# Kernel optimization log

Measured on AMD Instinct MI355X. Metric: run time of the kernel, lower is better.

Reference implementation:

```python
import jax, jax.numpy as jnp
import numpy as np

NLAYER = 4
H = 0.1


def tv_norm(X, eps=1e-3):
    # mean-center and L2-normalize each channel over the node/edge dim
    X = X - jnp.mean(X, axis=1, keepdims=True)
    return X / jnp.sqrt(jnp.sum(X * X, axis=1, keepdims=True) + eps)


def setup_inputs() -> dict:
    key = jax.random.key(0)
    ks = jax.random.split(key, 12)
    nIn, nopenN, nopenE, nclose = 128, 128, 128, 128
    nN, nE = 50000, 500000
    xn = jax.random.normal(ks[0], (nIn, nN), dtype=jnp.float32)
    xe = jax.random.normal(ks[1], (nIn, nE), dtype=jnp.float32)
    iInd = jax.random.randint(ks[2], (nE,), 0, nN)
    jInd = jax.random.randint(ks[3], (nE,), 0, nN)
    KNopen = jax.random.uniform(ks[4], (nopenN, nIn), dtype=jnp.float32) * 0.1
    KEopen = jax.random.uniform(ks[5], (nopenE, nIn), dtype=jnp.float32) * 0.1
    KNclose = jax.random.uniform(ks[6], (nclose, nopenN), dtype=jnp.float32) * 0.1
    KEclose = jax.random.uniform(ks[7], (nclose, nopenE), dtype=jnp.float32) * 0.1
    KN = jax.random.uniform(ks[8], (NLAYER, nopenE, nopenN), dtype=jnp.float32) * 0.001
    KE = jax.random.uniform(ks[9], (NLAYER, nopenN, nopenE), dtype=jnp.float32) * 0.001
    return {"xn": xn, "xe": xe, "iInd": iInd, "jInd": jInd,
            "KNopen": KNopen, "KEopen": KEopen, "KNclose": KNclose,
            "KEclose": KEclose, "KN": KN, "KE": KE}


def reference(xn, xe, iInd, jInd, KNopen, KEopen, KNclose, KEclose, KN, KE):
    nN = xn.shape[1]

    def node_grad(x):           # [d, nN] -> [d, nE]
        return x[:, iInd] - x[:, jInd]

    def edge_div(e):            # [d, nE] -> [d, nN]
        z = jnp.zeros((e.shape[0], nN), dtype=e.dtype)
        return z.at[:, iInd].add(e).at[:, jInd].add(-e)

    xn = KNopen @ xn            # [nopenN, nN]
    xe = KEopen @ xe            # [nopenE, nE]
    for i in range(NLAYER):
        Ai = tv_norm(KN[i] @ node_grad(xn))          # [nopenE, nE]
        xe = xe + H * jax.nn.relu(Ai)
        Bi = tv_norm(jax.nn.relu(KE[i] @ edge_div(xe)))  # [nopenN, nN]
        xn = xn + H * jax.nn.relu(Bi)
    xn = KNclose @ xn
    xe = KNclose @ xe  # note: original code uses KNclose for xe as well
    return (xn, xe)
```

## Files before the change

kernel.cpp:

```cpp
#include <hip/hip_runtime.h>


#define HSTEP 0.1f
#define TVEPS 1e-3f

typedef __attribute__((ext_vector_type(8))) short short8v;
typedef __attribute__((ext_vector_type(4))) float f32x4;

__device__ inline float4 f4z() { return make_float4(0.f, 0.f, 0.f, 0.f); }

__device__ inline unsigned short f2bf(float x) {
  unsigned u = __float_as_uint(x);
  unsigned r = (u + 0x7fffu + ((u >> 16) & 1u)) >> 16;
  return (unsigned short)r;
}
__device__ inline float bf2f(unsigned short h) {
  return __uint_as_float(((unsigned)h) << 16);
}

__global__ __launch_bounds__(256) void pack6(const float* __restrict__ KNopen,
                                             const float* __restrict__ KEopen,
                                             const float* __restrict__ KN,
                                             unsigned short* __restrict__ dst) {
  const int idx = blockIdx.x * 256 + threadIdx.x;
  const int m = blockIdx.y;
  const int o = idx >> 7, k = idx & 127;
  const float* src;
  if (m == 0) src = KNopen;
  else if (m == 1) src = KEopen;
  else src = KN + (m - 2) * 16384;
  const float val = src[o * 128 + k];
  const unsigned short hi = f2bf(val);
  const unsigned short lo = f2bf(val - bf2f(hi));
  const int lane = (o & 15) + 16 * ((k >> 3) & 3);
  const int base =
      m * 32768 + (k >> 5) * 8192 + (o >> 4) * 512 + lane * 8 + (k & 7);
  dst[base] = hi;
  dst[base + 4096] = lo;
}

__global__ __launch_bounds__(256) void prep_close_w(
    const float* __restrict__ KNclose, const float* __restrict__ KEopen,
    unsigned short* __restrict__ Apack) {
  const int idx = blockIdx.x * 256 + threadIdx.x;
  const int p = idx >> 14, ok = idx & 16383;
  const int o = ok >> 7, k = ok & 127;
  float val;
  if (p == 0) {
    float s = 0.f;
    for (int m = 0; m < 128; ++m)
      s = fmaf(KNclose[o * 128 + m], KEopen[m * 128 + k], s);
    val = s;
  } else {
    val = KNclose[o * 128 + k];
  }
  const unsigned short hi = f2bf(val);
  const unsigned short lo = f2bf(val - bf2f(hi));
  const int chunk = p * 4 + (k >> 5);
  const int lane = (o & 15) + 16 * ((k >> 3) & 3);
  const int base = chunk * 8192 + (o >> 4) * 512 + lane * 8 + (k & 7);
  Apack[base] = hi;
  Apack[base + 4096] = lo;
}

__global__ __launch_bounds__(256, 2) void gemm_e_mfma(
    const float* __restrict__ X, const unsigned short* __restrict__ Wp,
    const int N, float* __restrict__ Yt) {
  __shared__ float4 Asf[1024];
  const int tid = threadIdx.x;
  const int l = tid & 63, w = tid >> 6;
  const int er = l & 15, kg = l >> 4;
  const long e0 = (long)blockIdx.x * 128;

  f32x4 acc[8][2];
#pragma unroll
  for (int of = 0; of < 8; ++of)
#pragma unroll
    for (int f = 0; f < 2; ++f) acc[of][f] = (f32x4){0.f, 0.f, 0.f, 0.f};

  long e_f[2];
  bool ev[2];
#pragma unroll
  for (int f = 0; f < 2; ++f) {
    long e = e0 + 32 * w + 16 * f + er;
    ev[f] = (e < N);
    e_f[f] = ev[f] ? e : (long)(N - 1);
  }

  const short8v* Ap = (const short8v*)Asf;

  for (int ks = 0; ks < 4; ++ks) {
    const float4* src = (const float4*)Wp + ks * 1024;
    __syncthreads();
    Asf[tid] = src[tid];
    Asf[tid + 256] = src[tid + 256];
    Asf[tid + 512] = src[tid + 512];
    Asf[tid + 768] = src[tid + 768];
    __syncthreads();

    short8v bh[2], bl[2];
#pragma unroll
    for (int f = 0; f < 2; ++f) {
      const float* col = X + e_f[f];
      const int kbase = 32 * ks + 8 * kg;
      float xv[8];
#pragma unroll
      for (int j = 0; j < 8; ++j) xv[j] = col[(long)(kbase + j) * N];
#pragma unroll
      for (int j = 0; j < 8; ++j) {
        const unsigned short h = f2bf(xv[j]);
        const unsigned short lo = f2bf(xv[j] - bf2f(h));
        bh[f][j] = (short)h;
        bl[f][j] = (short)lo;
      }
    }

#pragma unroll
    for (int of = 0; of < 8; ++of) {
      const short8v ah = Ap[of * 64 + l];
      const short8v al = Ap[512 + of * 64 + l];
#pragma unroll
      for (int f = 0; f < 2; ++f) {
        acc[of][f] =
            __builtin_amdgcn_mfma_f32_16x16x32_bf16(ah, bh[f], acc[of][f], 0, 0, 0);
        acc[of][f] =
            __builtin_amdgcn_mfma_f32_16x16x32_bf16(ah, bl[f], acc[of][f], 0, 0, 0);
        acc[of][f] =
            __builtin_amdgcn_mfma_f32_16x16x32_bf16(al, bh[f], acc[of][f], 0, 0, 0);
      }
    }
  }

#pragma unroll
  for (int of = 0; of < 8; ++of) {
#pragma unroll
    for (int f = 0; f < 2; ++f) {
      if (!ev[f]) continue;
      *(f32x4*)&Yt[e_f[f] * 128 + of * 16 + 4 * kg] = acc[of][f];
    }
  }
}

template <int MODE>
__global__ __launch_bounds__(256, 2) void gemm_n_mfma(
    const float* __restrict__ X, const unsigned short* __restrict__ Wp,
    const int N, float* __restrict__ Y) {
  __shared__ float4 Asf[1024];
  const int tid = threadIdx.x;
  const int l = tid & 63, w = tid >> 6;
  const int er = l & 15, kg = l >> 4;
  const long n0 = (long)blockIdx.x * 128;

  f32x4 acc[8][2];
#pragma unroll
  for (int of = 0; of < 8; ++of)
#pragma unroll
    for (int f = 0; f < 2; ++f) acc[of][f] = (f32x4){0.f, 0.f, 0.f, 0.f};

  long n_f[2];
  bool nv[2];
#pragma unroll
  for (int f = 0; f < 2; ++f) {
    long n = n0 + 32 * w + 16 * f + er;
    nv[f] = (n < N);
    n_f[f] = nv[f] ? n : (long)(N - 1);
  }

  const short8v* Ap = (const short8v*)Asf;

  for (int ks = 0; ks < 4; ++ks) {
    const float4* src = (const float4*)Wp + ks * 1024;
    __syncthreads();
    Asf[tid] = src[tid];
    Asf[tid + 256] = src[tid + 256];
    Asf[tid + 512] = src[tid + 512];
    Asf[tid + 768] = src[tid + 768];
    __syncthreads();

    short8v bh[2], bl[2];
#pragma unroll
    for (int f = 0; f < 2; ++f) {
      const float* row = X + n_f[f] * 128 + 32 * ks + 8 * kg;
      const float4 v0 = *(const float4*)row;
      const float4 v1 = *(const float4*)(row + 4);
      float xv[8] = {v0.x, v0.y, v0.z, v0.w, v1.x, v1.y, v1.z, v1.w};
#pragma unroll
      for (int j = 0; j < 8; ++j) {
        const unsigned short h = f2bf(xv[j]);
        const unsigned short lo = f2bf(xv[j] - bf2f(h));
        bh[f][j] = (short)h;
        bl[f][j] = (short)lo;
      }
    }

#pragma unroll
    for (int of = 0; of < 8; ++of) {
      const short8v ah = Ap[of * 64 + l];
      const short8v al = Ap[512 + of * 64 + l];
#pragma unroll
      for (int f = 0; f < 2; ++f) {
        acc[of][f] =
            __builtin_amdgcn_mfma_f32_16x16x32_bf16(ah, bh[f], acc[of][f], 0, 0, 0);
        acc[of][f] =
            __builtin_amdgcn_mfma_f32_16x16x32_bf16(ah, bl[f], acc[of][f], 0, 0, 0);
        acc[of][f] =
            __builtin_amdgcn_mfma_f32_16x16x32_bf16(al, bh[f], acc[of][f], 0, 0, 0);
      }
    }
  }

  if (MODE == 0) {
#pragma unroll
    for (int of = 0; of < 8; ++of) {
#pragma unroll
      for (int f = 0; f < 2; ++f) {
        if (!nv[f]) continue;
        *(f32x4*)&Y[n_f[f] * 128 + of * 16 + 4 * kg] = acc[of][f];
      }
    }
  } else {
#pragma unroll
    for (int of = 0; of < 8; ++of) {
#pragma unroll
      for (int f = 0; f < 2; ++f) {
        if (!nv[f]) continue;
#pragma unroll
        for (int r = 0; r < 4; ++r) {
          const long o = of * 16 + 4 * kg + r;
          Y[o * N + n_f[f]] = acc[of][f][r];
        }
      }
    }
  }
}

__global__ __launch_bounds__(256, 2) void gemm_n1(
    const float* __restrict__ X, const float* __restrict__ Kmat, const int N,
    float* __restrict__ Y, float* __restrict__ statS,
    float* __restrict__ statQ) {
  __shared__ float Xs[64 * 33];
  __shared__ float Ks[32 * 132];
  __shared__ float red[2 * 128 * 17];
  const int tid = threadIdx.x;
  const int ng = tid & 15, og = tid >> 4;
  const long n0 = (long)blockIdx.x * 64;

  float acc[4][8];
#pragma unroll
  for (int q = 0; q < 4; ++q)
#pragma unroll
    for (int j = 0; j < 8; ++j) acc[q][j] = 0.f;

  for (int kc = 0; kc < 128; kc += 32) {
#pragma unroll
    for (int i = 0; i < 2; ++i) {
      int f4i = tid + 256 * i;
      int n = f4i >> 3, c4 = (f4i & 7) << 2;
      long gn = n0 + n;
      float4 v = f4z();
      if (gn < N) v = *(const float4*)&X[gn * 128 + kc + c4];
      Xs[n * 33 + c4 + 0] = v.x;
      Xs[n * 33 + c4 + 1] = v.y;
      Xs[n * 33 + c4 + 2] = v.z;
      Xs[n * 33 + c4 + 3] = v.w;
    }
#pragma unroll
    for (int i = 0; i < 4; ++i) {
      int f4i = tid + 256 * i;
      int o = f4i >> 3, c4 = (f4i & 7) << 2;
      float4 v = *(const float4*)&Kmat[o * 128 + kc + c4];
      Ks[(c4 + 0) * 132 + o] = v.x;
      Ks[(c4 + 1) * 132 + o] = v.y;
      Ks[(c4 + 2) * 132 + o] = v.z;
      Ks[(c4 + 3) * 132 + o] = v.w;
    }
    __syncthreads();
#pragma unroll
    for (int kk = 0; kk < 32; ++kk) {
      float xv[4];
#pragma unroll
      for (int q = 0; q < 4; ++q) xv[q] = Xs[(4 * ng + q) * 33 + kk];
      const float4 k0 = *(const float4*)&Ks[kk * 132 + 8 * og];
      const float4 k1 = *(const float4*)&Ks[kk * 132 + 8 * og + 4];
      float kv[8] = {k0.x, k0.y, k0.z, k0.w, k1.x, k1.y, k1.z, k1.w};
#pragma unroll
      for (int q = 0; q < 4; ++q)
#pragma unroll
        for (int j = 0; j < 8; ++j) acc[q][j] = fmaf(xv[q], kv[j], acc[q][j]);
    }
    __syncthreads();
  }

#pragma unroll
  for (int q = 0; q < 4; ++q)
#pragma unroll
    for (int j = 0; j < 8; ++j) acc[q][j] = fmaxf(acc[q][j], 0.f);
#pragma unroll
  for (int q = 0; q < 4; ++q) {
    long n = n0 + 4 * ng + q;
    if (n < N) {
      *(float4*)&Y[n * 128 + 8 * og] =
          make_float4(acc[q][0], acc[q][1], acc[q][2], acc[q][3]);
      *(float4*)&Y[n * 128 + 8 * og + 4] =
          make_float4(acc[q][4], acc[q][5], acc[q][6], acc[q][7]);
    }
  }
  float* redS = red;
  float* redQ = red + 128 * 17;
#pragma unroll
  for (int j = 0; j < 8; ++j) {
    int o = 8 * og + j;
    float s = acc[0][j] + acc[1][j] + acc[2][j] + acc[3][j];
    float qq = acc[0][j] * acc[0][j] + acc[1][j] * acc[1][j] +
               acc[2][j] * acc[2][j] + acc[3][j] * acc[3][j];
    redS[o * 17 + ng] = s;
    redQ[o * 17 + ng] = qq;
  }
  __syncthreads();
  if (tid < 128) {
    float s = 0.f, qq = 0.f;
#pragma unroll
    for (int g = 0; g < 16; ++g) {
      s += redS[tid * 17 + g];
      qq += redQ[tid * 17 + g];
    }
    atomicAdd(&statS[tid], s);
    atomicAdd(&statQ[tid], qq);
  }
}

__global__ __launch_bounds__(256, 2) void close_edge_mfma(
    const float* __restrict__ xe, const float* __restrict__ Sacc,
    const unsigned short* __restrict__ Apack, const int nE,
    float* __restrict__ out) {
  __shared__ float4 Asf[1024];
  const int tid = threadIdx.x;
  const int l = tid & 63, w = tid >> 6;
  const int er = l & 15;
  const int kg = l >> 4;
  const long e0 = (long)blockIdx.x * 128;

  f32x4 acc[8][2];
#pragma unroll
  for (int of = 0; of < 8; ++of)
#pragma unroll
    for (int f = 0; f < 2; ++f) acc[of][f] = (f32x4){0.f, 0.f, 0.f, 0.f};

  long e_f[2];
  bool ev[2];
#pragma unroll
  for (int f = 0; f < 2; ++f) {
    long e = e0 + 32 * w + 16 * f + er;
    ev[f] = (e < nE);
    e_f[f] = ev[f] ? e : (long)(nE - 1);
  }

  const short8v* Ap = (const short8v*)Asf;

  for (int p = 0; p < 2; ++p) {
    for (int ks = 0; ks < 4; ++ks) {
      const float4* src = (const float4*)Apack + (p * 4 + ks) * 1024;
      __syncthreads();
      Asf[tid] = src[tid];
      Asf[tid + 256] = src[tid + 256];
      Asf[tid + 512] = src[tid + 512];
      Asf[tid + 768] = src[tid + 768];
      __syncthreads();

      short8v bh[2], bl[2];
#pragma unroll
      for (int f = 0; f < 2; ++f) {
        float xv[8];
        if (p == 0) {
          const float* col = xe + e_f[f];
          const int kbase = 32 * ks + 8 * kg;
#pragma unroll
          for (int j = 0; j < 8; ++j) xv[j] = col[(long)(kbase + j) * nE];
        } else {
          const float* row = Sacc + e_f[f] * 128 + 32 * ks + 8 * kg;
          const float4 v0 = *(const float4*)row;
          const float4 v1 = *(const float4*)(row + 4);
          xv[0] = v0.x; xv[1] = v0.y; xv[2] = v0.z; xv[3] = v0.w;
          xv[4] = v1.x; xv[5] = v1.y; xv[6] = v1.z; xv[7] = v1.w;
        }
#pragma unroll
        for (int j = 0; j < 8; ++j) {
          const unsigned short h = f2bf(xv[j]);
          const unsigned short lo = f2bf(xv[j] - bf2f(h));
          bh[f][j] = (short)h;
          bl[f][j] = (short)lo;
        }
      }

#pragma unroll
      for (int of = 0; of < 8; ++of) {
        const short8v ah = Ap[of * 64 + l];
        const short8v al = Ap[512 + of * 64 + l];
#pragma unroll
        for (int f = 0; f < 2; ++f) {
          acc[of][f] =
              __builtin_amdgcn_mfma_f32_16x16x32_bf16(ah, bh[f], acc[of][f], 0, 0, 0);
          acc[of][f] =
              __builtin_amdgcn_mfma_f32_16x16x32_bf16(ah, bl[f], acc[of][f], 0, 0, 0);
          acc[of][f] =
              __builtin_amdgcn_mfma_f32_16x16x32_bf16(al, bh[f], acc[of][f], 0, 0, 0);
        }
      }
    }
  }

#pragma unroll
  for (int of = 0; of < 8; ++of) {
#pragma unroll
    for (int f = 0; f < 2; ++f) {
      if (!ev[f]) continue;
      const long e = e_f[f];
#pragma unroll
      for (int r = 0; r < 4; ++r) {
        const long o = of * 16 + 4 * kg + r;
        out[o * nE + e] = acc[of][f][r];
      }
    }
  }
}

__global__ __launch_bounds__(256) void count_deg(const int* __restrict__ iInd,
                                                 const int* __restrict__ jInd,
                                                 const int nE,
                                                 int* __restrict__ cnt) {
  const int e = blockIdx.x * 256 + threadIdx.x;
  if (e >= nE) return;
  atomicAdd(&cnt[iInd[e]], 1);
  atomicAdd(&cnt[jInd[e]], 1);
}

__global__ __launch_bounds__(1024) void scan_rowptr(const int* __restrict__ cnt,
                                                    int* __restrict__ rp,
                                                    const int nN) {
  __shared__ int buf[1024];
  __shared__ int carry;
  const int tid = threadIdx.x;
  if (tid == 0) {
    carry = 0;
    rp[0] = 0;
  }
  __syncthreads();
  for (int base = 0; base < nN; base += 1024) {
    int idx = base + tid;
    int v = (idx < nN) ? cnt[idx] : 0;
    buf[tid] = v;
    __syncthreads();
    for (int off = 1; off < 1024; off <<= 1) {
      int t = (tid >= off) ? buf[tid - off] : 0;
      __syncthreads();
      buf[tid] += t;
      __syncthreads();
    }
    if (idx < nN) rp[idx + 1] = buf[tid] + carry;
    __syncthreads();
    if (tid == 0) carry += buf[1023];
    __syncthreads();
  }
}

__global__ __launch_bounds__(256) void fill_adj(const int* __restrict__ iInd,
                                                const int* __restrict__ jInd,
                                                const int nE,
                                                const int* __restrict__ rp,
                                                int* __restrict__ cur,
                                                int* __restrict__ adj,
                                                int* __restrict__ adjO) {
  const int e = blockIdx.x * 256 + threadIdx.x;
  if (e >= nE) return;
  const int ii = iInd[e], jj = jInd[e];
  int s1 = atomicAdd(&cur[ii], 1);
  adj[rp[ii] + s1] = (e << 1);
  adjO[rp[ii] + s1] = jj;
  int s2 = atomicAdd(&cur[jj], 1);
  adj[rp[jj] + s2] = (e << 1) | 1;
  adjO[rp[jj] + s2] = ii;
}

__global__ __launch_bounds__(256) void div_open(
    const float* __restrict__ E, const int* __restrict__ rp,
    const int* __restrict__ adj, float* __restrict__ Dacc, const int nN) {
  const int cg = threadIdx.x & 31, slot = threadIdx.x >> 5;
  const long n = (long)blockIdx.x * 8 + slot;
  if (n >= nN) return;
  const float4* E4 = (const float4*)E;
  float4 acc = f4z();
  const int b = rp[n], en = rp[n + 1];
  for (int k = b; k < en; ++k) {
    const int ent = adj[k];
    const long e = ent >> 1;
    const float4 v = E4[e * 32 + cg];
    if (ent & 1) {
      acc.x -= v.x; acc.y -= v.y; acc.z -= v.z; acc.w -= v.w;
    } else {
      acc.x += v.x; acc.y += v.y; acc.z += v.z; acc.w += v.w;
    }
  }
  ((float4*)Dacc)[n * 32 + cg] = acc;
}

__global__ __launch_bounds__(256) void div_fused(
    const float* __restrict__ W, const int* __restrict__ rp,
    const int* __restrict__ adj, const int* __restrict__ adjO,
    const float* __restrict__ mean, const float* __restrict__ rsig,
    float* __restrict__ Dacc, const int nN) {
  const int cg = threadIdx.x & 31, slot = threadIdx.x >> 5;
  const long n = (long)blockIdx.x * 8 + slot;
  if (n >= nN) return;
  const float4* W4 = (const float4*)W;
  const float4 mu = *(const float4*)&mean[cg * 4];
  const float4 sg = *(const float4*)&rsig[cg * 4];
  const float4 wn = W4[n * 32 + cg];
  float4 acc = ((const float4*)Dacc)[n * 32 + cg];
  const int b = rp[n], en = rp[n + 1];
  for (int k = b; k < en; ++k) {
    const float s = (adj[k] & 1) ? -1.f : 1.f;
    const long o = adjO[k];
    const float4 wo = W4[o * 32 + cg];
    const float t0 = fmaxf((s * (wn.x - wo.x) - mu.x) * sg.x, 0.f);
    const float t1 = fmaxf((s * (wn.y - wo.y) - mu.y) * sg.y, 0.f);
    const float t2 = fmaxf((s * (wn.z - wo.z) - mu.z) * sg.z, 0.f);
    const float t3 = fmaxf((s * (wn.w - wo.w) - mu.w) * sg.w, 0.f);
    const float sh = s * HSTEP;
    acc.x = fmaf(sh, t0, acc.x);
    acc.y = fmaf(sh, t1, acc.y);
    acc.z = fmaf(sh, t2, acc.z);
    acc.w = fmaf(sh, t3, acc.w);
  }
  ((float4*)Dacc)[n * 32 + cg] = acc;
}

__global__ __launch_bounds__(256) void compute_sacc(
    const float* __restrict__ Wb, const long lstr4,
    const int* __restrict__ iInd, const int* __restrict__ jInd, const int nE,
    const float* __restrict__ meanAll, const float* __restrict__ rsigAll,
    float* __restrict__ Sacc) {
  const int tid = threadIdx.x;
  const int cg = tid & 31, slot = tid >> 5;
  float4 mu[4], sg[4];
#pragma unroll
  for (int l = 0; l < 4; ++l) {
    mu[l] = *(const float4*)&meanAll[l * 128 + cg * 4];
    sg[l] = *(const float4*)&rsigAll[l * 128 + cg * 4];
  }
  const float4* W4 = (const float4*)Wb;
  float4* S4 = (float4*)Sacc;
  long start = (long)blockIdx.x * 512;
  long end = start + 512;
  if (end > nE) end = nE;
  for (long e = start + slot; e < end; e += 8) {
    const long ii = iInd[e], jj = jInd[e];
    float4 acc = f4z();
#pragma unroll
    for (int l = 0; l < 4; ++l) {
      const float4 wi = W4[l * lstr4 + ii * 32 + cg];
      const float4 wj = W4[l * lstr4 + jj * 32 + cg];
      acc.x += HSTEP * fmaxf(((wi.x - wj.x) - mu[l].x) * sg[l].x, 0.f);
      acc.y += HSTEP * fmaxf(((wi.y - wj.y) - mu[l].y) * sg[l].y, 0.f);
      acc.z += HSTEP * fmaxf(((wi.z - wj.z) - mu[l].z) * sg[l].z, 0.f);
      acc.w += HSTEP * fmaxf(((wi.w - wj.w) - mu[l].w) * sg[l].w, 0.f);
    }
    S4[e * 32 + cg] = acc;
  }
}

__global__ __launch_bounds__(256) void edge_pass1(
    const float* __restrict__ W, const int* __restrict__ iInd,
    const int* __restrict__ jInd, const int nE, float* __restrict__ statS,
    float* __restrict__ statQ) {
  __shared__ float4 rs[256];
  __shared__ float4 rq[256];
  const int tid = threadIdx.x;
  const int cg = tid & 31, slot = tid >> 5;
  const float4* W4 = (const float4*)W;
  float4 s = f4z(), q = f4z();
  long start = (long)blockIdx.x * 512;
  long end = start + 512;
  if (end > nE) end = nE;
  for (long e = start + slot; e < end; e += 8) {
    const int ii = iInd[e], jj = jInd[e];
    const float4 wi = W4[(long)ii * 32 + cg];
    const float4 wj = W4[(long)jj * 32 + cg];
    const float y0 = wi.x - wj.x, y1 = wi.y - wj.y;
    const float y2 = wi.z - wj.z, y3 = wi.w - wj.w;
    s.x += y0; s.y += y1; s.z += y2; s.w += y3;
    q.x = fmaf(y0, y0, q.x); q.y = fmaf(y1, y1, q.y);
    q.z = fmaf(y2, y2, q.z); q.w = fmaf(y3, y3, q.w);
  }
  rs[tid] = s;
  rq[tid] = q;
  __syncthreads();
  if (tid < 32) {
    float4 S = rs[tid], Q = rq[tid];
#pragma unroll
    for (int g = 1; g < 8; ++g) {
      float4 a = rs[tid + 32 * g], b = rq[tid + 32 * g];
      S.x += a.x; S.y += a.y; S.z += a.z; S.w += a.w;
      Q.x += b.x; Q.y += b.y; Q.z += b.z; Q.w += b.w;
    }
    atomicAdd(&statS[tid * 4 + 0], S.x);
    atomicAdd(&statS[tid * 4 + 1], S.y);
    atomicAdd(&statS[tid * 4 + 2], S.z);
    atomicAdd(&statS[tid * 4 + 3], S.w);
    atomicAdd(&statQ[tid * 4 + 0], Q.x);
    atomicAdd(&statQ[tid * 4 + 1], Q.y);
    atomicAdd(&statQ[tid * 4 + 2], Q.z);
    atomicAdd(&statQ[tid * 4 + 3], Q.w);
  }
}

__global__ void fin_stats(const float* __restrict__ S,
                          const float* __restrict__ Q, const float cnt,
                          float* __restrict__ mean, float* __restrict__ rsig) {
  const int c = threadIdx.x;
  const float mu = S[c] / cnt;
  const float var = Q[c] - cnt * mu * mu;
  mean[c] = mu;
  rsig[c] = rsqrtf(var + TVEPS);
}

__global__ __launch_bounds__(256) void apply_node(
    const float* __restrict__ R, const float* __restrict__ mean,
    const float* __restrict__ rsig, float* __restrict__ xnt,
    const long total4) {
  const long idx = (long)blockIdx.x * 256 + threadIdx.x;
  if (idx >= total4) return;
  const int o4 = (int)(idx & 31) * 4;
  const float4 m = *(const float4*)&mean[o4];
  const float4 s = *(const float4*)&rsig[o4];
  const float4 r = ((const float4*)R)[idx];
  float4 x = ((float4*)xnt)[idx];
  x.x += HSTEP * fmaxf((r.x - m.x) * s.x, 0.f);
  x.y += HSTEP * fmaxf((r.y - m.y) * s.y, 0.f);
  x.z += HSTEP * fmaxf((r.z - m.z) * s.z, 0.f);
  x.w += HSTEP * fmaxf((r.w - m.w) * s.w, 0.f);
  ((float4*)xnt)[idx] = x;
}

extern "C" void kernel_launch(void* const* d_in, const int* in_sizes, int n_in,
                              void* d_out, int out_size, void* d_ws,
                              size_t ws_size, hipStream_t stream) {
  const float* xn = (const float*)d_in[0];
  const float* xe = (const float*)d_in[1];
  const int* iInd = (const int*)d_in[2];
  const int* jInd = (const int*)d_in[3];
  const float* KNopen = (const float*)d_in[4];
  const float* KEopen = (const float*)d_in[5];
  const float* KNclose = (const float*)d_in[6];
  const float* KN = (const float*)d_in[8];
  const float* KE = (const float*)d_in[9];

  const int nN = in_sizes[0] / 128;
  const int nE = in_sizes[2];

  float* out_xn = (float*)d_out;
  float* out_xe = (float*)d_out + (size_t)128 * nN;

  float* ws = (float*)d_ws;
  size_t off = 0;
  float* Sacc = ws + off; off += (size_t)nE * 128;
  float* Dacc = ws + off; off += (size_t)nN * 128;
  float* xnt  = ws + off; off += (size_t)nN * 128;
  unsigned short* Apack = (unsigned short*)(ws + off); off += 32768;
  unsigned short* Wpack = (unsigned short*)(ws + off); off += 98304;
  float* stats = ws + off; off += 2048;
  float* statS = stats;        float* statQ = stats + 128;
  float* statS2 = stats + 256; float* statQ2 = stats + 384;
  float* meanN = stats + 512;  float* rsigN = stats + 640;
  float* meanEall = stats + 768;
  float* rsigEall = stats + 1280;
  int* rp   = (int*)(ws + off); off += (size_t)nN + 1 + 63;
  int* cnt  = (int*)(ws + off); off += nN;
  int* cur  = (int*)(ws + off); off += nN;
  int* adj  = (int*)(ws + off); off += (size_t)2 * nE;
  int* adjO = (int*)(ws + off); off += (size_t)2 * nE;
  float* Eopen = Sacc;

  float* Wb = out_xe;
  float* R  = out_xe + (size_t)4 * nN * 128;

  const int gN = (nN + 63) / 64;
  const int gNm = (nN + 127) / 128;
  const int gEm = (nE + 127) / 128;
  const int gP = (nE + 511) / 512;
  const int gEdge = (nE + 255) / 256;
  const int gGath = (nN + 7) / 8;
  const int gA = (int)(((long)nN * 32 + 255) / 256);
  const long lstr4 = (long)nN * 32;

  hipMemsetAsync(cnt, 0, (size_t)nN * sizeof(int), stream);
  hipMemsetAsync(cur, 0, (size_t)nN * sizeof(int), stream);
  count_deg<<<gEdge, 256, 0, stream>>>(iInd, jInd, nE, cnt);
  scan_rowptr<<<1, 1024, 0, stream>>>(cnt, rp, nN);
  fill_adj<<<gEdge, 256, 0, stream>>>(iInd, jInd, nE, rp, cur, adj, adjO);

  pack6<<<dim3(64, 6), 256, 0, stream>>>(KNopen, KEopen, KN, Wpack);
  prep_close_w<<<128, 256, 0, stream>>>(KNclose, KEopen, Apack);

  gemm_e_mfma<<<gNm, 256, 0, stream>>>(xn, Wpack, nN, xnt);
  gemm_e_mfma<<<gEm, 256, 0, stream>>>(xe, Wpack + 32768, nE, Eopen);
  div_open<<<gGath, 256, 0, stream>>>(Eopen, rp, adj, Dacc, nN);

  for (int layer = 0; layer < 4; ++layer) {
    float* Wl = Wb + (size_t)layer * nN * 128;
    float* meanE = meanEall + 128 * layer;
    float* rsigE = rsigEall + 128 * layer;
    hipMemsetAsync(stats, 0, 512 * sizeof(float), stream);
    gemm_n_mfma<0><<<gNm, 256, 0, stream>>>(
        xnt, Wpack + (size_t)(2 + layer) * 32768, nN, Wl);
    edge_pass1<<<gP, 256, 0, stream>>>(Wl, iInd, jInd, nE, statS, statQ);
    fin_stats<<<1, 128, 0, stream>>>(statS, statQ, (float)nE, meanE, rsigE);
    div_fused<<<gGath, 256, 0, stream>>>(Wl, rp, adj, adjO, meanE, rsigE,
                                         Dacc, nN);
    gemm_n1<<<gN, 256, 0, stream>>>(Dacc, KE + layer * 16384, nN, R, statS2,
                                    statQ2);
    fin_stats<<<1, 128, 0, stream>>>(statS2, statQ2, (float)nN, meanN, rsigN);
    apply_node<<<gA, 256, 0, stream>>>(R, meanN, rsigN, xnt, (long)nN * 32);
  }

  compute_sacc<<<gP, 256, 0, stream>>>(Wb, lstr4, iInd, jInd, nE, meanEall,
                                       rsigEall, Sacc);
  gemm_n_mfma<2><<<gNm, 256, 0, stream>>>(xnt, Apack + 32768, nN, out_xn);
  close_edge_mfma<<<gEm, 256, 0, stream>>>(xe, Sacc, Apack, nE, out_xe);
}
```

Baseline: 2.596 ms.

## Compute edge stats via node-degree algebra and CSR walk; CSR-based final edge accumulation

Edge-gradient mean and variance are rebuilt algebraically: sum uses signed degree times node features, and sum of squares uses degree-weighted squared node features minus twice a cross term gathered along CSR forward edges. This replaces the per-edge two-gather pass with a per-node walk that reads the own row once and gathers one neighbor per edge. The final Sacc computation is also moved to a CSR walk so the source row stays in registers while the writes scatter by edge id. The variance formula via E[x^2]-mu^2 risks cancellation in fp32, and the scattered writes may hurt coalescing.

```diff
diff --git a/kernel.cpp b/kernel.cpp
--- a/kernel.cpp
+++ b/kernel.cpp
@@ -427,11 +427,14 @@
 __global__ __launch_bounds__(256) void count_deg(const int* __restrict__ iInd,
                                                  const int* __restrict__ jInd,
                                                  const int nE,
-                                                 int* __restrict__ cnt) {
+                                                 int* __restrict__ cnt,
+                                                 int* __restrict__ degD) {
   const int e = blockIdx.x * 256 + threadIdx.x;
   if (e >= nE) return;
   atomicAdd(&cnt[iInd[e]], 1);
   atomicAdd(&cnt[jInd[e]], 1);
+  atomicAdd(&degD[iInd[e]], 1);
+  atomicAdd(&degD[jInd[e]], -1);
 }
 
 __global__ __launch_bounds__(1024) void scan_rowptr(const int* __restrict__ cnt,
@@ -501,6 +504,73 @@
     }
   }
   ((float4*)Dacc)[n * 32 + cg] = acc;
+}
+
+__global__ __launch_bounds__(256) void stats_walk(
+    const float* __restrict__ W, const int* __restrict__ rp,
+    const int* __restrict__ adj, const int* __restrict__ adjO,
+    const int* __restrict__ degS, const int* __restrict__ degD, const int nN,
+    float* __restrict__ statS, float* __restrict__ statQ2,
+    float* __restrict__ statX) {
+  __shared__ float4 red[3 * 256];
+  const int tid = threadIdx.x;
+  const int cg = tid & 31, slot = tid >> 5;
+  const float4* W4 = (const float4*)W;
+  float4 S = f4z(), Q = f4z(), X = f4z();
+  const long n0 = (long)blockIdx.x * 64;
+  for (int t = 0; t < 8; ++t) {
+    const long n = n0 + t * 8 + slot;
+    if (n >= nN) break;
+    const float dD = (float)degD[n];
+    const float dS = (float)degS[n];
+    const float4 wn = W4[n * 32 + cg];
+    S.x = fmaf(dD, wn.x, S.x);
+    S.y = fmaf(dD, wn.y, S.y);
+    S.z = fmaf(dD, wn.z, S.z);
+    S.w = fmaf(dD, wn.w, S.w);
+    Q.x = fmaf(dS * wn.x, wn.x, Q.x);
+    Q.y = fmaf(dS * wn.y, wn.y, Q.y);
+    Q.z = fmaf(dS * wn.z, wn.z, Q.z);
+    Q.w = fmaf(dS * wn.w, wn.w, Q.w);
+    const int b = rp[n], en = rp[n + 1];
+    for (int k = b; k < en; ++k) {
+      if (adj[k] & 1) continue;
+      const long o = adjO[k];
+      const float4 wo = W4[o * 32 + cg];
+      X.x = fmaf(wn.x, wo.x, X.x);
+      X.y = fmaf(wn.y, wo.y, X.y);
+      X.z = fmaf(wn.z, wo.z, X.z);
+      X.w = fmaf(wn.w, wo.w, X.w);
+    }
+  }
+  red[tid] = S;
+  red[256 + tid] = Q;
+  red[512 + tid] = X;
+  __syncthreads();
+  if (tid < 32) {
+    float4 aS = red[tid], aQ = red[256 + tid], aX = red[512 + tid];
+#pragma unroll
+    for (int g = 1; g < 8; ++g) {
+      const float4 bS = red[32 * g + tid];
+      const float4 bQ = red[256 + 32 * g + tid];
+      const float4 bX = red[512 + 32 * g + tid];
+      aS.x += bS.x; aS.y += bS.y; aS.z += bS.z; aS.w += bS.w;
+      aQ.x += bQ.x; aQ.y += bQ.y; aQ.z += bQ.z; aQ.w += bQ.w;
+      aX.x += bX.x; aX.y += bX.y; aX.z += bX.z; aX.w += bX.w;
+    }
+    atomicAdd(&statS[tid * 4 + 0], aS.x);
+    atomicAdd(&statS[tid * 4 + 1], aS.y);
+    atomicAdd(&statS[tid * 4 + 2], aS.z);
+    atomicAdd(&statS[tid * 4 + 3], aS.w);
+    atomicAdd(&statQ2[tid * 4 + 0], aQ.x);
+    atomicAdd(&statQ2[tid * 4 + 1], aQ.y);
+    atomicAdd(&statQ2[tid * 4 + 2], aQ.z);
+    atomicAdd(&statQ2[tid * 4 + 3], aQ.w);
+    atomicAdd(&statX[tid * 4 + 0], aX.x);
+    atomicAdd(&statX[tid * 4 + 1], aX.y);
+    atomicAdd(&statX[tid * 4 + 2], aX.z);
+    atomicAdd(&statX[tid * 4 + 3], aX.w);
+  }
 }
 
 __global__ __launch_bounds__(256) void div_fused(
@@ -534,83 +604,52 @@
   ((float4*)Dacc)[n * 32 + cg] = acc;
 }
 
-__global__ __launch_bounds__(256) void compute_sacc(
-    const float* __restrict__ Wb, const long lstr4,
-    const int* __restrict__ iInd, const int* __restrict__ jInd, const int nE,
+__global__ __launch_bounds__(256) void compute_sacc_csr(
+    const float* __restrict__ Wb, const long lstr4, const int* __restrict__ rp,
+    const int* __restrict__ adj, const int* __restrict__ adjO, const int nN,
     const float* __restrict__ meanAll, const float* __restrict__ rsigAll,
     float* __restrict__ Sacc) {
-  const int tid = threadIdx.x;
-  const int cg = tid & 31, slot = tid >> 5;
-  float4 mu[4], sg[4];
+  const int cg = threadIdx.x & 31, slot = threadIdx.x >> 5;
+  const long n = (long)blockIdx.x * 8 + slot;
+  if (n >= nN) return;
+  const float4* W4 = (const float4*)Wb;
+  float4 mu[4], sg[4], wn[4];
 #pragma unroll
   for (int l = 0; l < 4; ++l) {
     mu[l] = *(const float4*)&meanAll[l * 128 + cg * 4];
     sg[l] = *(const float4*)&rsigAll[l * 128 + cg * 4];
-  }
-  const float4* W4 = (const float4*)Wb;
+    wn[l] = W4[l * lstr4 + n * 32 + cg];
+  }
   float4* S4 = (float4*)Sacc;
-  long start = (long)blockIdx.x * 512;
-  long end = start + 512;
-  if (end > nE) end = nE;
-  for (long e = start + slot; e < end; e += 8) {
-    const long ii = iInd[e], jj = jInd[e];
+  const int b = rp[n], en = rp[n + 1];
+  for (int k = b; k < en; ++k) {
+    const int ent = adj[k];
+    if (ent & 1) continue;
+    const long e = ent >> 1;
+    const long j = adjO[k];
     float4 acc = f4z();
 #pragma unroll
     for (int l = 0; l < 4; ++l) {
-      const float4 wi = W4[l * lstr4 + ii * 32 + cg];
-      const float4 wj = W4[l * lstr4 + jj * 32 + cg];
-      acc.x += HSTEP * fmaxf(((wi.x - wj.x) - mu[l].x) * sg[l].x, 0.f);
-      acc.y += HSTEP * fmaxf(((wi.y - wj.y) - mu[l].y) * sg[l].y, 0.f);
-      acc.z += HSTEP * fmaxf(((wi.z - wj.z) - mu[l].z) * sg[l].z, 0.f);
-      acc.w += HSTEP * fmaxf(((wi.w - wj.w) - mu[l].w) * sg[l].w, 0.f);
+      const float4 wj = W4[l * lstr4 + j * 32 + cg];
+      acc.x += HSTEP * fmaxf(((wn[l].x - wj.x) - mu[l].x) * sg[l].x, 0.f);
+      acc.y += HSTEP * fmaxf(((wn[l].y - wj.y) - mu[l].y) * sg[l].y, 0.f);
+      acc.z += HSTEP * fmaxf(((wn[l].z - wj.z) - mu[l].z) * sg[l].z, 0.f);
+      acc.w += HSTEP * fmaxf(((wn[l].w - wj.w) - mu[l].w) * sg[l].w, 0.f);
     }
     S4[e * 32 + cg] = acc;
   }
 }
 
-__global__ __launch_bounds__(256) void edge_pass1(
-    const float* __restrict__ W, const int* __restrict__ iInd,
-    const int* __restrict__ jInd, const int nE, float* __restrict__ statS,
-    float* __restrict__ statQ) {
-  __shared__ float4 rs[256];
-  __shared__ float4 rq[256];
-  const int tid = threadIdx.x;
-  const int cg = tid & 31, slot = tid >> 5;
-  const float4* W4 = (const float4*)W;
-  float4 s = f4z(), q = f4z();
-  long start = (long)blockIdx.x * 512;
-  long end = start + 512;
-  if (end > nE) end = nE;
-  for (long e = start + slot; e < end; e += 8) {
-    const int ii = iInd[e], jj = jInd[e];
-    const float4 wi = W4[(long)ii * 32 + cg];
-    const float4 wj = W4[(long)jj * 32 + cg];
-    const float y0 = wi.x - wj.x, y1 = wi.y - wj.y;
-    const float y2 = wi.z - wj.z, y3 = wi.w - wj.w;
-    s.x += y0; s.y += y1; s.z += y2; s.w += y3;
-    q.x = fmaf(y0, y0, q.x); q.y = fmaf(y1, y1, q.y);
-    q.z = fmaf(y2, y2, q.z); q.w = fmaf(y3, y3, q.w);
-  }
-  rs[tid] = s;
-  rq[tid] = q;
-  __syncthreads();
-  if (tid < 32) {
-    float4 S = rs[tid], Q = rq[tid];
-#pragma unroll
-    for (int g = 1; g < 8; ++g) {
-      float4 a = rs[tid + 32 * g], b = rq[tid + 32 * g];
-      S.x += a.x; S.y += a.y; S.z += a.z; S.w += a.w;
-      Q.x += b.x; Q.y += b.y; Q.z += b.z; Q.w += b.w;
-    }
-    atomicAdd(&statS[tid * 4 + 0], S.x);
-    atomicAdd(&statS[tid * 4 + 1], S.y);
-    atomicAdd(&statS[tid * 4 + 2], S.z);
-    atomicAdd(&statS[tid * 4 + 3], S.w);
-    atomicAdd(&statQ[tid * 4 + 0], Q.x);
-    atomicAdd(&statQ[tid * 4 + 1], Q.y);
-    atomicAdd(&statQ[tid * 4 + 2], Q.z);
-    atomicAdd(&statQ[tid * 4 + 3], Q.w);
-  }
+__global__ void fin_statsE(const float* __restrict__ S,
+                           const float* __restrict__ Q2,
+                           const float* __restrict__ X, const float cnt,
+                           float* __restrict__ mean, float* __restrict__ rsig) {
+  const int c = threadIdx.x;
+  const float mu = S[c] / cnt;
+  const float q = Q2[c] - 2.f * X[c];
+  const float var = q - cnt * mu * mu;
+  mean[c] = mu;
+  rsig[c] = rsqrtf(var + TVEPS);
 }
 
 __global__ void fin_stats(const float* __restrict__ S,
@@ -668,14 +707,16 @@
   unsigned short* Apack = (unsigned short*)(ws + off); off += 32768;
   unsigned short* Wpack = (unsigned short*)(ws + off); off += 98304;
   float* stats = ws + off; off += 2048;
-  float* statS = stats;        float* statQ = stats + 128;
-  float* statS2 = stats + 256; float* statQ2 = stats + 384;
-  float* meanN = stats + 512;  float* rsigN = stats + 640;
-  float* meanEall = stats + 768;
-  float* rsigEall = stats + 1280;
+  float* statS = stats;         float* statQ2 = stats + 128;
+  float* statX = stats + 256;
+  float* statS2 = stats + 384;  float* statQn = stats + 512;
+  float* meanN = stats + 640;   float* rsigN = stats + 768;
+  float* meanEall = stats + 896;
+  float* rsigEall = stats + 1408;
   int* rp   = (int*)(ws + off); off += (size_t)nN + 1 + 63;
   int* cnt  = (int*)(ws + off); off += nN;
   int* cur  = (int*)(ws + off); off += nN;
+  int* degD = (int*)(ws + off); off += nN;
   int* adj  = (int*)(ws + off); off += (size_t)2 * nE;
   int* adjO = (int*)(ws + off); off += (size_t)2 * nE;
   float* Eopen = Sacc;
@@ -686,15 +727,16 @@
   const int gN = (nN + 63) / 64;
   const int gNm = (nN + 127) / 128;
   const int gEm = (nE + 127) / 128;
-  const int gP = (nE + 511) / 512;
   const int gEdge = (nE + 255) / 256;
   const int gGath = (nN + 7) / 8;
+  const int gStat = (nN + 63) / 64;
   const int gA = (int)(((long)nN * 32 + 255) / 256);
   const long lstr4 = (long)nN * 32;
 
   hipMemsetAsync(cnt, 0, (size_t)nN * sizeof(int), stream);
   hipMemsetAsync(cur, 0, (size_t)nN * sizeof(int), stream);
-  count_deg<<<gEdge, 256, 0, stream>>>(iInd, jInd, nE, cnt);
+  hipMemsetAsync(degD, 0, (size_t)nN * sizeof(int), stream);
+  count_deg<<<gEdge, 256, 0, stream>>>(iInd, jInd, nE, cnt, degD);
   scan_rowptr<<<1, 1024, 0, stream>>>(cnt, rp, nN);
   fill_adj<<<gEdge, 256, 0, stream>>>(iInd, jInd, nE, rp, cur, adj, adjO);
 
@@ -709,21 +751,23 @@
     float* Wl = Wb + (size_t)layer * nN * 128;
     float* meanE = meanEall + 128 * layer;
     float* rsigE = rsigEall + 128 * layer;
-    hipMemsetAsync(stats, 0, 512 * sizeof(float), stream);
+    hipMemsetAsync(stats, 0, 640 * sizeof(float), stream);
     gemm_n_mfma<0><<<gNm, 256, 0, stream>>>(
         xnt, Wpack + (size_t)(2 + layer) * 32768, nN, Wl);
-    edge_pass1<<<gP, 256, 0, stream>>>(Wl, iInd, jInd, nE, statS, statQ);
-    fin_stats<<<1, 128, 0, stream>>>(statS, statQ, (float)nE, meanE, rsigE);
+    stats_walk<<<gStat, 256, 0, stream>>>(Wl, rp, adj, adjO, cnt, degD, nN,
+                                          statS, statQ2, statX);
+    fin_statsE<<<1, 128, 0, stream>>>(statS, statQ2, statX, (float)nE, meanE,
+                                      rsigE);
     div_fused<<<gGath, 256, 0, stream>>>(Wl, rp, adj, adjO, meanE, rsigE,
                                          Dacc, nN);
     gemm_n1<<<gN, 256, 0, stream>>>(Dacc, KE + layer * 16384, nN, R, statS2,
-                                    statQ2);
-    fin_stats<<<1, 128, 0, stream>>>(statS2, statQ2, (float)nN, meanN, rsigN);
+                                    statQn);
+    fin_stats<<<1, 128, 0, stream>>>(statS2, statQn, (float)nN, meanN, rsigN);
     apply_node<<<gA, 256, 0, stream>>>(R, meanN, rsigN, xnt, (long)nN * 32);
   }
 
-  compute_sacc<<<gP, 256, 0, stream>>>(Wb, lstr4, iInd, jInd, nE, meanEall,
-                                       rsigEall, Sacc);
+  compute_sacc_csr<<<gGath, 256, 0, stream>>>(Wb, lstr4, rp, adj, adjO, nN,
+                                              meanEall, rsigEall, Sacc);
   gemm_n_mfma<2><<<gNm, 256, 0, stream>>>(xnt, Apack + 32768, nN, out_xn);
   close_edge_mfma<<<gEm, 256, 0, stream>>>(xe, Sacc, Apack, nE, out_xe);
 }
```

After: 2.665 ms. 2.7% more time.
